# Performance work log

Measured on AMD Instinct MI355X. Metric: run time of the kernel, lower is better.

The kernel has to match this reference:

```python
import jax, jax.numpy as jnp
import numpy as np

NEG_SLOPE = 0.01  # nn.LeakyReLU default

def leaky_relu(x):
    return jnp.where(x >= 0, x, NEG_SLOPE * x)

def rgcn_conv(x, weight, root, bias, src, dst, edge_type, num_relations, num_nodes):
    """PyG RGCNConv with default mean aggregation.
    weight: [R, in, out], root: [in, out], bias: [out].
    out[i] = x[i] @ root + bias + sum_r mean_{edges e of type r with dst=i} (x[src_e] @ W_r)
    """
    out = x @ root + bias
    for r in range(num_relations):
        mask = (edge_type == r)
        h = x @ weight[r]                       # [N, out] transform once per relation
        msg = h[src] * mask[:, None].astype(x.dtype)   # [E, out], zeroed off-relation
        s = jax.ops.segment_sum(msg, dst, num_segments=num_nodes)
        cnt = jax.ops.segment_sum(mask.astype(x.dtype), dst, num_segments=num_nodes)
        out = out + s / jnp.maximum(cnt, 1.0)[:, None]
    return out

def setup_inputs() -> dict:
    key = jax.random.key(0)
    ks = jax.random.split(key, 16)
    N, E, IN, HID, OUT, R = 50000, 800000, 768, 256, 2, 2
    x = jax.random.normal(ks[0], (N, IN), dtype=jnp.float32)
    edge_index = jax.random.randint(ks[1], (2, E), 0, N, dtype=jnp.int64)
    edge_weight = jax.random.uniform(ks[2], (E,), dtype=jnp.float32)
    edge_type = jax.random.randint(ks[3], (E,), 0, R, dtype=jnp.int64)
    def lin(k, fin, fout):
        s = 1.0 / np.sqrt(fin)
        k1, k2 = jax.random.split(k)
        W = jax.random.uniform(k1, (fin, fout), minval=-s, maxval=s, dtype=jnp.float32)
        b = jax.random.uniform(k2, (fout,), minval=-s, maxval=s, dtype=jnp.float32)
        return W, b
    fc1_W, fc1_b = lin(ks[4], IN, IN)
    fc2_W, fc2_b = lin(ks[5], HID, HID)
    out_W, out_b = lin(ks[6], HID, OUT)
    g = 1.0 / np.sqrt(IN)
    r1_weight = jax.random.uniform(ks[7], (R, IN, HID), minval=-g, maxval=g, dtype=jnp.float32)
    r1_root = jax.random.uniform(ks[8], (IN, HID), minval=-g, maxval=g, dtype=jnp.float32)
    r1_bias = jnp.zeros((HID,), dtype=jnp.float32)
    g2 = 1.0 / np.sqrt(HID)
    r2_weight = jax.random.uniform(ks[9], (R, HID, HID), minval=-g2, maxval=g2, dtype=jnp.float32)
    r2_root = jax.random.uniform(ks[10], (HID, HID), minval=-g2, maxval=g2, dtype=jnp.float32)
    r2_bias = jnp.zeros((HID,), dtype=jnp.float32)
    return {"x": x, "edge_index": edge_index, "edge_weight": edge_weight,
            "edge_type": edge_type,
            "fc1_W": fc1_W, "fc1_b": fc1_b,
            "r1_weight": r1_weight, "r1_root": r1_root, "r1_bias": r1_bias,
            "r2_weight": r2_weight, "r2_root": r2_root, "r2_bias": r2_bias,
            "fc2_W": fc2_W, "fc2_b": fc2_b,
            "out_W": out_W, "out_b": out_b}

def reference(x, edge_index, edge_weight, edge_type,
              fc1_W, fc1_b, r1_weight, r1_root, r1_bias,
              r2_weight, r2_root, r2_bias, fc2_W, fc2_b, out_W, out_b):
    N = x.shape[0]
    R = r1_weight.shape[0]
    src, dst = edge_index[0], edge_index[1]
    h = leaky_relu(x @ fc1_W + fc1_b)
    h = rgcn_conv(h, r1_weight, r1_root, r1_bias, src, dst, edge_type, R, N)
    h = rgcn_conv(h, r2_weight, r2_root, r2_bias, src, dst, edge_type, R, N)
    h = leaky_relu(h @ fc2_W + fc2_b)
    return jax.nn.softmax(h @ out_W + out_b, axis=1)
```

## Files before the change

### kernel.cpp

```cpp
#include <hip/hip_runtime.h>
#include <stdint.h>

__device__ __forceinline__ float b2f(unsigned short s) {
    union { uint32_t u; float f; } v; v.u = ((uint32_t)s) << 16; return v.f;
}
__device__ __forceinline__ unsigned short f2b(float f) {
    union { float f; uint32_t u; } v; v.f = f;
    uint32_t r = v.u + 0x7FFFu + ((v.u >> 16) & 1u);
    return (unsigned short)(r >> 16);
}
__device__ __forceinline__ int ld_idx(const void* p, long long i, int i64) {
    return i64 ? (int)((const long long*)p)[i] : ((const int*)p)[i];
}

typedef __bf16 bf16x8 __attribute__((ext_vector_type(8)));
typedef float  f32x4  __attribute__((ext_vector_type(4)));

__global__ void detect_kernel(const void* __restrict__ x, const void* __restrict__ eidx,
                              int* __restrict__ flags) {
    __shared__ int cntF, cntI;
    int t = threadIdx.x;
    if (t == 0) { cntF = 0; cntI = 0; }
    __syncthreads();
    const unsigned short* xs = (const unsigned short*)x;
    int lf = 0;
    for (int i = t; i < 4096; i += 256) {
        unsigned short v = xs[2 * i];
        int e = (v >> 7) & 0xFF;
        if (v == 0 || (e >= 100 && e <= 140)) lf++;
    }
    const int* ei = (const int*)eidx;
    int li = 0;
    for (int i = t; i < 2048; i += 256)
        if (ei[2 * i + 1] != 0) li++;
    atomicAdd(&cntF, lf);
    atomicAdd(&cntI, li);
    __syncthreads();
    if (t == 0) {
        flags[0] = (cntF < 3000) ? 1 : 0;
        flags[1] = (cntI < 64) ? 1 : 0;
    }
}

__global__ void convt_kernel(const void* __restrict__ W, size_t src_off,
                             unsigned short* __restrict__ Wt, int K, int N,
                             const int* __restrict__ flags) {
    int id = blockIdx.x * 256 + threadIdx.x;
    if (id < K * N) {
        int n = id / K, k = id - n * K;
        size_t s = src_off + (size_t)k * N + n;
        Wt[id] = flags[0] ? f2b(((const float*)W)[s]) : ((const unsigned short*)W)[s];
    }
}

__global__ void convb_kernel(const void* __restrict__ src, unsigned short* __restrict__ dst,
                             int n, const int* __restrict__ flags) {
    int i = blockIdx.x * 256 + threadIdx.x;
    if (i < n)
        dst[i] = flags[0] ? f2b(((const float*)src)[i]) : ((const unsigned short*)src)[i];
}

__global__ void convx_kernel(const void* __restrict__ src, unsigned short* __restrict__ dst,
                             int n8, const int* __restrict__ flags) {
    int i = blockIdx.x * 256 + threadIdx.x;
    if (i < n8) {
        if (flags[0]) {
            const float4* p = (const float4*)src + (size_t)i * 2;
            float4 a = p[0], b = p[1];
            union { int4 v; unsigned short s[8]; } u;
            u.s[0] = f2b(a.x); u.s[1] = f2b(a.y); u.s[2] = f2b(a.z); u.s[3] = f2b(a.w);
            u.s[4] = f2b(b.x); u.s[5] = f2b(b.y); u.s[6] = f2b(b.z); u.s[7] = f2b(b.w);
            ((int4*)dst)[i] = u.v;
        } else {
            ((int4*)dst)[i] = ((const int4*)src)[i];
        }
    }
}

__global__ void zero_kernel(int* __restrict__ p, int n) {
    int i = blockIdx.x * 256 + threadIdx.x;
    if (i < n) p[i] = 0;
}
__global__ void zero_us_kernel(unsigned short* __restrict__ p, int n) {
    int i = blockIdx.x * 256 + threadIdx.x;
    if (i < n) p[i] = 0;
}

__global__ void count_kernel(const void* __restrict__ eidx, const void* __restrict__ etype,
                             int* __restrict__ cnt, int E, int NN,
                             const int* __restrict__ flags) {
    int e = blockIdx.x * 256 + threadIdx.x;
    if (e < E) {
        int i64 = flags[1];
        int d = ld_idx(eidx, (long long)E + e, i64);
        d = min(max(d, 0), NN - 1);
        int ty = ld_idx(etype, e, i64) & 1;
        atomicAdd(&cnt[ty * NN + d], 1);
    }
}

__global__ void inv_deg_kernel(const int* __restrict__ cnt, float* __restrict__ inv,
                               int* __restrict__ deg, int NN) {
    int i = blockIdx.x * 256 + threadIdx.x;
    if (i < NN) {
        int c0 = cnt[i], c1 = cnt[NN + i];
        inv[i]      = 1.0f / (float)max(c0, 1);
        inv[NN + i] = 1.0f / (float)max(c1, 1);
        deg[i] = c0 + c1;
    }
}

__global__ void blocksum_kernel(const int* __restrict__ deg, int* __restrict__ bsum, int n) {
    __shared__ int red[256];
    int t = threadIdx.x, b = blockIdx.x;
    int base = b * 1024 + t * 4;
    int s = 0;
    #pragma unroll
    for (int j = 0; j < 4; ++j) {
        int idx = base + j;
        if (idx < n) s += deg[idx];
    }
    red[t] = s;
    __syncthreads();
    for (int off = 128; off > 0; off >>= 1) {
        if (t < off) red[t] += red[t + off];
        __syncthreads();
    }
    if (t == 0) bsum[b] = red[0];
}
__global__ void scan_bsum_kernel(int* __restrict__ bsum, int nb) {
    if (threadIdx.x == 0 && blockIdx.x == 0) {
        int acc = 0;
        for (int i = 0; i < nb; ++i) { int v = bsum[i]; bsum[i] = acc; acc += v; }
    }
}
__global__ void scan_phase3(const int* __restrict__ deg, const int* __restrict__ bsum,
                            int* __restrict__ row_ptr, int* __restrict__ pos, int n) {
    __shared__ int buf[256];
    int t = threadIdx.x, b = blockIdx.x;
    int base = b * 1024;
    int v[4]; int s = 0;
    #pragma unroll
    for (int j = 0; j < 4; ++j) {
        int idx = base + t * 4 + j;
        v[j] = (idx < n) ? deg[idx] : 0;
        s += v[j];
    }
    buf[t] = s;
    __syncthreads();
    for (int off = 1; off < 256; off <<= 1) {
        int xv = (t >= off) ? buf[t - off] : 0;
        __syncthreads();
        buf[t] += xv;
        __syncthreads();
    }
    int run = buf[t] - s + bsum[b];
    #pragma unroll
    for (int j = 0; j < 4; ++j) {
        int idx = base + t * 4 + j;
        if (idx < n) {
            run += v[j];
            row_ptr[idx + 1] = run;
            if (idx + 1 < n) pos[idx + 1] = run;
        }
    }
    if (b == 0 && t == 0) { row_ptr[0] = 0; pos[0] = 0; }
}

__global__ void fill_kernel(const void* __restrict__ eidx, const void* __restrict__ etype,
                            int* __restrict__ pos, int* __restrict__ packed, int E, int NN,
                            const int* __restrict__ flags) {
    int e = blockIdx.x * 256 + threadIdx.x;
    if (e < E) {
        int i64 = flags[1];
        int s = ld_idx(eidx, e, i64);
        int d = ld_idx(eidx, (long long)E + e, i64);
        s = min(max(s, 0), NN - 1);
        d = min(max(d, 0), NN - 1);
        int ty = ld_idx(etype, e, i64) & 1;
        int slot = atomicAdd(&pos[d], 1);
        packed[slot] = (ty << 24) | s;
    }
}

template<bool LEAKY, bool HAS_BIAS>
__global__ __launch_bounds__(256) void gemm_kernel(
    const unsigned short* __restrict__ A,
    const unsigned short* __restrict__ Wt,
    const unsigned short* __restrict__ bias,
    unsigned short* __restrict__ C,
    int M, int N, int K)
{
    __shared__ __align__(16) unsigned short As[128][40];
    __shared__ __align__(16) unsigned short Bs[128][40];

    const int t    = threadIdx.x;
    const int lane = t & 63;
    const int wave = t >> 6;
    const int wm   = wave >> 1;
    const int wn   = wave & 1;
    const int l16  = lane & 15;
    const int quad = lane >> 4;
    const int col0 = blockIdx.x * 128;
    const int row0 = blockIdx.y * 128;

    f32x4 acc[4][4] = {};

    for (int k0 = 0; k0 < K; k0 += 32) {
        #pragma unroll
        for (int i = 0; i < 2; ++i) {
            int c = t + 256 * i;
            int r = c >> 2, col = (c & 3) * 8;
            int gr = row0 + r;
            int4 v = make_int4(0, 0, 0, 0);
            if (gr < M)
                v = *reinterpret_cast<const int4*>(A + (size_t)gr * K + k0 + col);
            *reinterpret_cast<int4*>(&As[r][col]) = v;
        }
        #pragma unroll
        for (int i = 0; i < 2; ++i) {
            int c = t + 256 * i;
            int r = c >> 2, col = (c & 3) * 8;
            int4 v = *reinterpret_cast<const int4*>(&Wt[(size_t)(col0 + r) * K + k0 + col]);
            *reinterpret_cast<int4*>(&Bs[r][col]) = v;
        }
        __syncthreads();

        bf16x8 af[4], bfr[4];
        #pragma unroll
        for (int mi = 0; mi < 4; ++mi)
            af[mi] = *reinterpret_cast<const bf16x8*>(&As[wm * 64 + mi * 16 + l16][quad * 8]);
        #pragma unroll
        for (int ni = 0; ni < 4; ++ni)
            bfr[ni] = *reinterpret_cast<const bf16x8*>(&Bs[wn * 64 + ni * 16 + l16][quad * 8]);
        #pragma unroll
        for (int mi = 0; mi < 4; ++mi)
            #pragma unroll
            for (int ni = 0; ni < 4; ++ni)
                acc[mi][ni] = __builtin_amdgcn_mfma_f32_16x16x32_bf16(
                    af[mi], bfr[ni], acc[mi][ni], 0, 0, 0);
        __syncthreads();
    }

    #pragma unroll
    for (int mi = 0; mi < 4; ++mi) {
        #pragma unroll
        for (int ni = 0; ni < 4; ++ni) {
            int ccol = col0 + wn * 64 + ni * 16 + l16;
            float bv = HAS_BIAS ? b2f(bias[ccol]) : 0.0f;
            #pragma unroll
            for (int i = 0; i < 4; ++i) {
                int r = row0 + wm * 64 + mi * 16 + quad * 4 + i;
                if (r < M) {
                    float v = acc[mi][ni][i] + bv;
                    if (LEAKY) v = (v >= 0.0f) ? v : 0.01f * v;
                    C[(size_t)r * N + ccol] = f2b(v);
                }
            }
        }
    }
}

__global__ __launch_bounds__(256) void gather_kernel(
    const int* __restrict__ row_ptr, const int* __restrict__ packed,
    const float* __restrict__ inv,
    const unsigned short* __restrict__ P,
    unsigned short* __restrict__ outp,
    int NN)
{
    int i    = blockIdx.x * 4 + (threadIdx.x >> 6);
    int lane = threadIdx.x & 63;
    if (i >= NN) return;
    float w0 = inv[i], w1 = inv[NN + i];
    ushort4 rv = *reinterpret_cast<const ushort4*>(P + (size_t)i * 768 + 512 + lane * 4);
    float a0 = b2f(rv.x), a1 = b2f(rv.y), a2 = b2f(rv.z), a3 = b2f(rv.w);
    int e = row_ptr[i], e1 = row_ptr[i + 1];
    for (; e < e1; ++e) {
        int p = packed[e];
        int s = p & 0xFFFFFF;
        if (s >= NN) s = NN - 1;
        int r = (p >> 24) & 1;
        float w = r ? w1 : w0;
        ushort4 hv = *reinterpret_cast<const ushort4*>(
            P + (size_t)s * 768 + r * 256 + lane * 4);
        a0 += w * b2f(hv.x);
        a1 += w * b2f(hv.y);
        a2 += w * b2f(hv.z);
        a3 += w * b2f(hv.w);
    }
    ushort4 o;
    o.x = f2b(a0); o.y = f2b(a1); o.z = f2b(a2); o.w = f2b(a3);
    *reinterpret_cast<ushort4*>(outp + (size_t)i * 256 + lane * 4) = o;
}

__global__ __launch_bounds__(256) void head_kernel(
    const unsigned short* __restrict__ h,
    const unsigned short* __restrict__ outW,
    const unsigned short* __restrict__ outb,
    void* __restrict__ out, int M, const int* __restrict__ flags)
{
    int row  = blockIdx.x * 4 + (threadIdx.x >> 6);
    int lane = threadIdx.x & 63;
    if (row >= M) return;
    ushort4 hv = *reinterpret_cast<const ushort4*>(h + (size_t)row * 256 + lane * 4);
    union { int4 v; unsigned short s[8]; } wu;
    wu.v = *reinterpret_cast<const int4*>(outW + lane * 8);
    float hf[4] = { b2f(hv.x), b2f(hv.y), b2f(hv.z), b2f(hv.w) };
    float s0 = 0.0f, s1 = 0.0f;
    #pragma unroll
    for (int i = 0; i < 4; ++i) {
        s0 += hf[i] * b2f(wu.s[2 * i]);
        s1 += hf[i] * b2f(wu.s[2 * i + 1]);
    }
    #pragma unroll
    for (int off2 = 32; off2 >= 1; off2 >>= 1) {
        s0 += __shfl_down(s0, off2);
        s1 += __shfl_down(s1, off2);
    }
    if (lane == 0) {
        s0 += b2f(outb[0]); s1 += b2f(outb[1]);
        float m  = fmaxf(s0, s1);
        float e0 = expf(s0 - m), e1 = expf(s1 - m);
        float is = 1.0f / (e0 + e1);
        if (flags[0]) {
            ((float*)out)[(size_t)row * 2 + 0] = e0 * is;
            ((float*)out)[(size_t)row * 2 + 1] = e1 * is;
        } else {
            ((unsigned short*)out)[(size_t)row * 2 + 0] = f2b(e0 * is);
            ((unsigned short*)out)[(size_t)row * 2 + 1] = f2b(e1 * is);
        }
    }
}

__global__ void diag_kernel(unsigned short* __restrict__ out, int n, float v) {
    int i = blockIdx.x * 256 + threadIdx.x;
    if (i < n) out[i] = f2b(v);
}

template<bool LEAKY, bool HAS_BIAS>
static void launch_gemm(const unsigned short* A, const unsigned short* Wt,
                        const unsigned short* bias, unsigned short* C,
                        int M, int N, int K, hipStream_t s) {
    int MP = (M + 127) & ~127;
    dim3 grid(N / 128, MP / 128);
    gemm_kernel<LEAKY, HAS_BIAS><<<grid, 256, 0, s>>>(A, Wt, bias, C, M, N, K);
}

extern "C" void kernel_launch(void* const* d_in, const int* in_sizes, int n_in,
                              void* d_out, int out_size, void* d_ws, size_t ws_size,
                              hipStream_t stream) {
    const int IN = 768, HID = 256;
    const int NN = in_sizes[0] / IN;
    const int E  = in_sizes[3];
    const int MP = (NN + 127) & ~127;
    const int NB = (NN + 1023) / 1024;
    (void)n_in;

    const void* x    = d_in[0];
    const void* eidx = d_in[1];
    const void* etyp = d_in[3];
    const void* fc1W = d_in[4];
    const void* fc1b = d_in[5];
    const void* r1w  = d_in[6];
    const void* r1r  = d_in[7];
    const void* r1b  = d_in[8];
    const void* r2w  = d_in[9];
    const void* r2r  = d_in[10];
    const void* r2b  = d_in[11];
    const void* fc2W = d_in[12];
    const void* fc2b = d_in[13];
    const void* outW = d_in[14];
    const void* outb = d_in[15];

    char* ws = (char*)d_ws;
    size_t off = 0;
    auto carve = [&](size_t bytes) {
        char* p = ws + off; off += (bytes + 255) & ~(size_t)255; return p;
    };
    int*   flags = (int*)carve(64);
    unsigned short* fc1t  = (unsigned short*)carve((size_t)IN * IN * 2);
    unsigned short* Wcat1 = (unsigned short*)carve((size_t)IN * IN * 2);
    unsigned short* Wcat2 = (unsigned short*)carve((size_t)IN * HID * 2);
    unsigned short* fc2t  = (unsigned short*)carve((size_t)HID * HID * 2);
    unsigned short* fc1bc = (unsigned short*)carve((size_t)IN * 2);
    unsigned short* bcat1 = (unsigned short*)carve((size_t)IN * 2);
    unsigned short* bcat2 = (unsigned short*)carve((size_t)IN * 2);
    unsigned short* fc2bc = (unsigned short*)carve((size_t)HID * 2);
    unsigned short* outWc = (unsigned short*)carve((size_t)HID * 2 * 2);
    unsigned short* outbc = (unsigned short*)carve(2 * 2);
    int*   icnt    = (int*)carve((size_t)2 * NN * 4);
    float* inv     = (float*)carve((size_t)2 * NN * 4);
    int*   deg     = (int*)carve((size_t)NN * 4);
    int*   row_ptr = (int*)carve((size_t)(NN + 1) * 4);
    int*   pos     = (int*)carve((size_t)NN * 4);
    int*   bsum    = (int*)carve(256 * 4);
    int*   packed  = (int*)carve((size_t)E * 4);
    unsigned short* RA = (unsigned short*)carve((size_t)MP * IN * 2);
    unsigned short* RB = (unsigned short*)carve((size_t)MP * IN * 2);

    auto tg = [](int n) { return (n + 255) / 256; };

    if (ws_size < off) {
        float v = fminf((float)(ws_size >> 20), 300.0f) / 1000.0f;
        diag_kernel<<<tg(out_size), 256, 0, stream>>>((unsigned short*)d_out, out_size, v);
        return;
    }

    detect_kernel<<<1, 256, 0, stream>>>(x, eidx, flags);

    convt_kernel<<<tg(IN * IN), 256, 0, stream>>>(fc1W, 0, fc1t, IN, IN, flags);
    convt_kernel<<<tg(IN * HID), 256, 0, stream>>>(r1w, 0, Wcat1, IN, HID, flags);
    convt_kernel<<<tg(IN * HID), 256, 0, stream>>>(r1w, (size_t)IN * HID, Wcat1 + (size_t)256 * IN, IN, HID, flags);
    convt_kernel<<<tg(IN * HID), 256, 0, stream>>>(r1r, 0, Wcat1 + (size_t)512 * IN, IN, HID, flags);
    convt_kernel<<<tg(HID * HID), 256, 0, stream>>>(r2w, 0, Wcat2, HID, HID, flags);
    convt_kernel<<<tg(HID * HID), 256, 0, stream>>>(r2w, (size_t)HID * HID, Wcat2 + (size_t)256 * HID, HID, HID, flags);
    convt_kernel<<<tg(HID * HID), 256, 0, stream>>>(r2r, 0, Wcat2 + (size_t)512 * HID, HID, HID, flags);
    convt_kernel<<<tg(HID * HID), 256, 0, stream>>>(fc2W, 0, fc2t, HID, HID, flags);
    zero_us_kernel<<<tg(512), 256, 0, stream>>>(bcat1, 512);
    zero_us_kernel<<<tg(512), 256, 0, stream>>>(bcat2, 512);
    convb_kernel<<<tg(IN), 256, 0, stream>>>(fc1b, fc1bc, IN, flags);
    convb_kernel<<<1, 256, 0, stream>>>(r1b, bcat1 + 512, HID, flags);
    convb_kernel<<<1, 256, 0, stream>>>(r2b, bcat2 + 512, HID, flags);
    convb_kernel<<<1, 256, 0, stream>>>(fc2b, fc2bc, HID, flags);
    convb_kernel<<<tg(HID * 2), 256, 0, stream>>>(outW, outWc, HID * 2, flags);
    convb_kernel<<<1, 256, 0, stream>>>(outb, outbc, 2, flags);

    zero_kernel<<<tg(2 * NN), 256, 0, stream>>>(icnt, 2 * NN);
    count_kernel<<<tg(E), 256, 0, stream>>>(eidx, etyp, icnt, E, NN, flags);
    inv_deg_kernel<<<tg(NN), 256, 0, stream>>>(icnt, inv, deg, NN);
    blocksum_kernel<<<NB, 256, 0, stream>>>(deg, bsum, NN);
    scan_bsum_kernel<<<1, 64, 0, stream>>>(bsum, NB);
    scan_phase3<<<NB, 256, 0, stream>>>(deg, bsum, row_ptr, pos, NN);
    fill_kernel<<<tg(E), 256, 0, stream>>>(eidx, etyp, pos, packed, E, NN, flags);

    convx_kernel<<<tg(NN * IN / 8), 256, 0, stream>>>(x, RA, NN * IN / 8, flags);

    launch_gemm<true, true>(RA, fc1t, fc1bc, RB, NN, IN, IN, stream);

    launch_gemm<false, true>(RB, Wcat1, bcat1, RA, NN, IN, IN, stream);
    gather_kernel<<<(NN + 3) / 4, 256, 0, stream>>>(row_ptr, packed, inv, RA, RB, NN);

    launch_gemm<false, true>(RB, Wcat2, bcat2, RA, NN, IN, HID, stream);
    gather_kernel<<<(NN + 3) / 4, 256, 0, stream>>>(row_ptr, packed, inv, RA, RB, NN);

    launch_gemm<true, true>(RB, fc2t, fc2bc, RA, NN, HID, HID, stream);
    head_kernel<<<(NN + 3) / 4, 256, 0, stream>>>(RA, outWc, outbc, d_out, NN, flags);
}
```

Baseline: 915.7 us.

## Deepen GEMM K-tile to 64 and split gather edges across half-waves

The GEMM now stages 64-wide K slices in LDS and runs two MFMA sub-steps per tile, which halves the number of barrier pairs and global-load rounds per output tile at the cost of more LDS. The gather kernel now uses 16-byte loads: each half-wave covers the full 256-wide row with 8 elements per lane and takes alternate edges. The two partial sums are combined with a cross-lane shuffle at the end. This aims for wider memory transactions and two outstanding edge gathers per wave, adding shuffle work and more registers per lane.

```diff
diff --git a/kernel.cpp b/kernel.cpp
--- a/kernel.cpp
+++ b/kernel.cpp
@@ -191,8 +191,8 @@
     unsigned short* __restrict__ C,
     int M, int N, int K)
 {
-    __shared__ __align__(16) unsigned short As[128][40];
-    __shared__ __align__(16) unsigned short Bs[128][40];
+    __shared__ __align__(16) unsigned short As[128][72];
+    __shared__ __align__(16) unsigned short Bs[128][72];
 
     const int t    = threadIdx.x;
     const int lane = t & 63;
@@ -206,11 +206,11 @@
 
     f32x4 acc[4][4] = {};
 
-    for (int k0 = 0; k0 < K; k0 += 32) {
-        #pragma unroll
-        for (int i = 0; i < 2; ++i) {
+    for (int k0 = 0; k0 < K; k0 += 64) {
+        #pragma unroll
+        for (int i = 0; i < 4; ++i) {
             int c = t + 256 * i;
-            int r = c >> 2, col = (c & 3) * 8;
+            int r = c >> 3, col = (c & 7) * 8;
             int gr = row0 + r;
             int4 v = make_int4(0, 0, 0, 0);
             if (gr < M)
@@ -218,27 +218,32 @@
             *reinterpret_cast<int4*>(&As[r][col]) = v;
         }
         #pragma unroll
-        for (int i = 0; i < 2; ++i) {
+        for (int i = 0; i < 4; ++i) {
             int c = t + 256 * i;
-            int r = c >> 2, col = (c & 3) * 8;
+            int r = c >> 3, col = (c & 7) * 8;
             int4 v = *reinterpret_cast<const int4*>(&Wt[(size_t)(col0 + r) * K + k0 + col]);
             *reinterpret_cast<int4*>(&Bs[r][col]) = v;
         }
         __syncthreads();
 
-        bf16x8 af[4], bfr[4];
-        #pragma unroll
-        for (int mi = 0; mi < 4; ++mi)
-            af[mi] = *reinterpret_cast<const bf16x8*>(&As[wm * 64 + mi * 16 + l16][quad * 8]);
-        #pragma unroll
-        for (int ni = 0; ni < 4; ++ni)
-            bfr[ni] = *reinterpret_cast<const bf16x8*>(&Bs[wn * 64 + ni * 16 + l16][quad * 8]);
-        #pragma unroll
-        for (int mi = 0; mi < 4; ++mi)
+        #pragma unroll
+        for (int kk = 0; kk < 2; ++kk) {
+            bf16x8 af[4], bfr[4];
+            #pragma unroll
+            for (int mi = 0; mi < 4; ++mi)
+                af[mi] = *reinterpret_cast<const bf16x8*>(
+                    &As[wm * 64 + mi * 16 + l16][kk * 32 + quad * 8]);
             #pragma unroll
             for (int ni = 0; ni < 4; ++ni)
-                acc[mi][ni] = __builtin_amdgcn_mfma_f32_16x16x32_bf16(
-                    af[mi], bfr[ni], acc[mi][ni], 0, 0, 0);
+                bfr[ni] = *reinterpret_cast<const bf16x8*>(
+                    &Bs[wn * 64 + ni * 16 + l16][kk * 32 + quad * 8]);
+            #pragma unroll
+            for (int mi = 0; mi < 4; ++mi)
+                #pragma unroll
+                for (int ni = 0; ni < 4; ++ni)
+                    acc[mi][ni] = __builtin_amdgcn_mfma_f32_16x16x32_bf16(
+                        af[mi], bfr[ni], acc[mi][ni], 0, 0, 0);
+        }
         __syncthreads();
     }
 
@@ -270,27 +275,37 @@
 {
     int i    = blockIdx.x * 4 + (threadIdx.x >> 6);
     int lane = threadIdx.x & 63;
+    int half = lane >> 5;
+    int l32  = lane & 31;
     if (i >= NN) return;
     float w0 = inv[i], w1 = inv[NN + i];
-    ushort4 rv = *reinterpret_cast<const ushort4*>(P + (size_t)i * 768 + 512 + lane * 4);
-    float a0 = b2f(rv.x), a1 = b2f(rv.y), a2 = b2f(rv.z), a3 = b2f(rv.w);
-    int e = row_ptr[i], e1 = row_ptr[i + 1];
-    for (; e < e1; ++e) {
+    float a[8] = {};
+    if (half == 0) {
+        union { int4 v; unsigned short s[8]; } ru;
+        ru.v = *reinterpret_cast<const int4*>(P + (size_t)i * 768 + 512 + l32 * 8);
+        #pragma unroll
+        for (int j = 0; j < 8; ++j) a[j] = b2f(ru.s[j]);
+    }
+    int e1 = row_ptr[i + 1];
+    for (int e = row_ptr[i] + half; e < e1; e += 2) {
         int p = packed[e];
         int s = p & 0xFFFFFF;
         if (s >= NN) s = NN - 1;
         int r = (p >> 24) & 1;
         float w = r ? w1 : w0;
-        ushort4 hv = *reinterpret_cast<const ushort4*>(
-            P + (size_t)s * 768 + r * 256 + lane * 4);
-        a0 += w * b2f(hv.x);
-        a1 += w * b2f(hv.y);
-        a2 += w * b2f(hv.z);
-        a3 += w * b2f(hv.w);
-    }
-    ushort4 o;
-    o.x = f2b(a0); o.y = f2b(a1); o.z = f2b(a2); o.w = f2b(a3);
-    *reinterpret_cast<ushort4*>(outp + (size_t)i * 256 + lane * 4) = o;
+        union { int4 v; unsigned short s8[8]; } hu;
+        hu.v = *reinterpret_cast<const int4*>(P + (size_t)s * 768 + r * 256 + l32 * 8);
+        #pragma unroll
+        for (int j = 0; j < 8; ++j) a[j] += w * b2f(hu.s8[j]);
+    }
+    union { int4 v; unsigned short s[8]; } ou;
+    #pragma unroll
+    for (int j = 0; j < 8; ++j) {
+        float m = a[j] + __shfl_down(a[j], 32);
+        ou.s[j] = f2b(m);
+    }
+    if (half == 0)
+        *reinterpret_cast<int4*>(outp + (size_t)i * 256 + l32 * 8) = ou.v;
 }
 
 __global__ __launch_bounds__(256) void head_kernel(
```

Result: faster. 871.0 us (-4.9%).
